# Kernel tuning notes

Hardware: AMD Instinct MI355X
Metric: run time of the kernel (lower is better)

## Reference

```python
import jax, jax.numpy as jnp
import numpy as np

N, M, D_MODEL, H, D_K, D_V = 2048, 2048, 1024, 16, 64, 64


def setup_inputs() -> dict:
    key = jax.random.key(0)
    ks = jax.random.split(key, 12)
    s = D_MODEL ** -0.5
    Q = jax.random.normal(ks[0], (N, D_MODEL), dtype=jnp.float32)
    K = jax.random.normal(ks[1], (M, D_MODEL), dtype=jnp.float32)
    V = jax.random.normal(ks[2], (M, D_MODEL), dtype=jnp.float32)
    mask = jnp.ones((N, M), dtype=bool)  # unused by the original forward
    # stacked per-head Linear params (torch Linear: y = x @ W.T + b); here stored as (H, in, out)
    Wq = jax.random.normal(ks[3], (H, D_MODEL, D_K), dtype=jnp.float32) * s
    bq = jax.random.normal(ks[4], (H, D_K), dtype=jnp.float32) * 0.01
    Wk = jax.random.normal(ks[5], (H, D_MODEL, D_K), dtype=jnp.float32) * s
    bk = jax.random.normal(ks[6], (H, D_K), dtype=jnp.float32) * 0.01
    Wv = jax.random.normal(ks[7], (H, D_MODEL, D_V), dtype=jnp.float32) * s
    bv = jax.random.normal(ks[8], (H, D_V), dtype=jnp.float32) * 0.01
    Wo = jax.random.normal(ks[9], (H * D_V, D_MODEL), dtype=jnp.float32) * ((H * D_V) ** -0.5)
    bo = jax.random.normal(ks[10], (D_MODEL,), dtype=jnp.float32) * 0.01
    return dict(Q=Q, K=K, V=V, mask=mask, Wq=Wq, bq=bq, Wk=Wk, bk=bk,
                Wv=Wv, bv=bv, Wo=Wo, bo=bo)


def reference(Q, K, V, mask, Wq, bq, Wk, bk, Wv, bv, Wo, bo):
    # per-head projections, batched over heads (h)
    Qh = jnp.einsum('nd,hdk->hnk', Q, Wq) + bq[:, None, :]  # (H, n, d_k)
    Kh = jnp.einsum('md,hdk->hmk', K, Wk) + bk[:, None, :]  # (H, m, d_k)
    Vh = jnp.einsum('md,hdv->hmv', V, Wv) + bv[:, None, :]  # (H, m, d_v)
    # faithful to source: scale d_k**-0.5 is applied AFTER the softmax
    scores = jnp.einsum('hnk,hmk->hnm', Qh, Kh)             # (H, n, m)
    attn = jax.nn.softmax(scores, axis=-1) * (D_K ** -0.5)
    heads = jnp.einsum('hnm,hmv->hnv', attn, Vh)            # (H, n, d_v)
    concat = jnp.transpose(heads, (1, 0, 2)).reshape(heads.shape[1], H * D_V)
    return concat @ Wo + bo                                  # (n, d_model)
```

## Files before the change

kernel.cpp:

```cpp
#include <hip/hip_runtime.h>

#define N_TOK 2048
#define DMODEL 1024
#define NH 16
#define DK 64
#define SOFF 48.0f

typedef __attribute__((ext_vector_type(8))) short bfrag;
typedef __attribute__((ext_vector_type(4))) float f32x4;
typedef __attribute__((ext_vector_type(16))) float f32x16;
typedef __attribute__((ext_vector_type(4))) unsigned u32x4;

__device__ __forceinline__ unsigned short f2bf(float f) {
    unsigned u = __builtin_bit_cast(unsigned, f);
    u += 0x7FFFu + ((u >> 16) & 1u);
    return (unsigned short)(u >> 16);
}
__device__ __forceinline__ float bf2f(unsigned short u) {
    unsigned x = ((unsigned)u) << 16;
    return __builtin_bit_cast(float, x);
}
__device__ __forceinline__ unsigned cvtpk(float lo, float hi) {
    unsigned r;
    asm volatile("v_cvt_pk_bf16_f32 %0, %1, %2" : "=v"(r) : "v"(lo), "v"(hi));
    return r;
}

__device__ __forceinline__ int swz(int row, int b) {
    return row * 128 + (b ^ ((row & 7) << 4));
}

__device__ __forceinline__ void gload16(const void* g, void* l) {
    __builtin_amdgcn_global_load_lds(
        (__attribute__((address_space(1))) void*)g,
        (__attribute__((address_space(3))) void*)l,
        16, 0, 0);
}

__global__ __launch_bounds__(256) void prep_kernel(
    const float* __restrict__ Qin, const float* __restrict__ Kin, const float* __restrict__ Vin,
    const float* __restrict__ Wq_, const float* __restrict__ Wk_, const float* __restrict__ Wv_,
    const float* __restrict__ Wo_,
    unsigned short* __restrict__ AhQ, unsigned short* __restrict__ AhK, unsigned short* __restrict__ AhV,
    unsigned short* __restrict__ WthQ, unsigned short* __restrict__ WthK, unsigned short* __restrict__ WthV,
    unsigned short* __restrict__ WoT)
{
    const int bid = blockIdx.x;
    const int tid = threadIdx.x;
    __shared__ float lds[64][65];

    if (bid < 3072) {
        const int z = bid >> 10, x = bid & 1023;
        const float* src = (z == 0) ? Qin : (z == 1) ? Kin : Vin;
        unsigned short* dh = (z == 0) ? AhQ : (z == 1) ? AhK : AhV;
        size_t base = ((size_t)x * 256 + tid) * 8;
        float4 a = *reinterpret_cast<const float4*>(src + base);
        float4 b = *reinterpret_cast<const float4*>(src + base + 4);
        float f[8] = {a.x, a.y, a.z, a.w, b.x, b.y, b.z, b.w};
        unsigned short hb[8];
        #pragma unroll
        for (int i = 0; i < 8; ++i) hb[i] = f2bf(f[i]);
        *reinterpret_cast<uint4*>(dh + base) = *reinterpret_cast<const uint4*>(hb);
    } else if (bid < 3840) {
        const int t = bid - 3072;
        const int z = t >> 8, rem = t & 255;
        const int h = rem >> 4, dt = rem & 15;
        const float* W = (z == 0) ? Wq_ : (z == 1) ? Wk_ : Wv_;
        unsigned short* oh = (z == 0) ? WthQ : (z == 1) ? WthK : WthV;

        {
            int rr = tid >> 2, c4 = (tid & 3) * 16;
            const float* src = W + ((size_t)h * DMODEL + dt * 64 + rr) * DK + c4;
            #pragma unroll
            for (int i = 0; i < 4; ++i) {
                float4 v = *reinterpret_cast<const float4*>(src + i * 4);
                lds[rr][c4 + i * 4 + 0] = v.x;
                lds[rr][c4 + i * 4 + 1] = v.y;
                lds[rr][c4 + i * 4 + 2] = v.z;
                lds[rr][c4 + i * 4 + 3] = v.w;
            }
        }
        __syncthreads();
        {
            int kk_ = tid >> 2, d4 = (tid & 3) * 16;
            unsigned short hb[16];
            #pragma unroll
            for (int i = 0; i < 16; ++i) hb[i] = f2bf(lds[d4 + i][kk_]);
            size_t o = (size_t)(h * 64 + kk_) * DMODEL + dt * 64 + d4;
            *reinterpret_cast<uint4*>(oh + o)     = *reinterpret_cast<const uint4*>(hb);
            *reinterpret_cast<uint4*>(oh + o + 8) = *reinterpret_cast<const uint4*>(hb + 8);
        }
    } else {
        const int t = bid - 3840;
        const int dt = t >> 4, jt = t & 15;
        {
            int rr = tid >> 2, c4 = (tid & 3) * 16;
            const float* src = Wo_ + (size_t)(dt * 64 + rr) * DMODEL + jt * 64 + c4;
            #pragma unroll
            for (int i = 0; i < 4; ++i) {
                float4 v = *reinterpret_cast<const float4*>(src + i * 4);
                lds[rr][c4 + i * 4 + 0] = v.x;
                lds[rr][c4 + i * 4 + 1] = v.y;
                lds[rr][c4 + i * 4 + 2] = v.z;
                lds[rr][c4 + i * 4 + 3] = v.w;
            }
        }
        __syncthreads();
        {
            int jj = tid >> 2, d4 = (tid & 3) * 16;
            unsigned short hb[16];
            #pragma unroll
            for (int i = 0; i < 16; ++i) hb[i] = f2bf(lds[d4 + i][jj]);
            size_t o = (size_t)(jt * 64 + jj) * DMODEL + dt * 64 + d4;
            *reinterpret_cast<uint4*>(WoT + o)     = *reinterpret_cast<const uint4*>(hb);
            *reinterpret_cast<uint4*>(WoT + o + 8) = *reinterpret_cast<const uint4*>(hb + 8);
        }
    }
}

__global__ __launch_bounds__(256) void proj_kernel(
    const unsigned short* __restrict__ AhQ, const unsigned short* __restrict__ AhK, const unsigned short* __restrict__ AhV,
    const unsigned short* __restrict__ WthQ, const unsigned short* __restrict__ WthK, const unsigned short* __restrict__ WthV,
    const float* __restrict__ bq_, const float* __restrict__ bk_, const float* __restrict__ bv_,
    unsigned short* __restrict__ Qhh,
    unsigned short* __restrict__ Khh,
    unsigned short* __restrict__ Vt)
{
    const int z = blockIdx.z;
    const unsigned short* Ah = (z == 0) ? AhK : (z == 1) ? AhQ : AhV;
    const unsigned short* Bh = (z == 0) ? WthK : (z == 1) ? WthQ : WthV;
    const float* bias = (z == 0) ? bk_ : (z == 1) ? bq_ : bv_;

    __shared__ alignas(16) unsigned char sAh[16384];
    __shared__ alignas(16) unsigned char sBh[16384];

    const int tid = threadIdx.x;
    const int lane = tid & 63;
    const int w = tid >> 6;
    const int wm = w >> 1, wn = w & 1;
    const int g = lane >> 4, li = lane & 15;

    const int row0 = blockIdx.x * 128;
    const int col0 = blockIdx.y * 128;

    f32x4 acc[4][4];
    #pragma unroll
    for (int m = 0; m < 4; ++m)
        #pragma unroll
        for (int n = 0; n < 4; ++n) acc[m][n] = f32x4{0.f, 0.f, 0.f, 0.f};

    for (int kt = 0; kt < DMODEL; kt += 64) {
        __syncthreads();
        #pragma unroll
        for (int p = 0; p < 4; ++p) {
            int chunk = p * 256 + tid;
            int r = chunk >> 3, cc = chunk & 7;
            int cs = (cc * 8) ^ ((r & 7) << 3);
            int ldso = (p * 256 + w * 64) * 16;
            gload16(Ah + (size_t)(row0 + r) * DMODEL + kt + cs, sAh + ldso);
            gload16(Bh + (size_t)(col0 + r) * DMODEL + kt + cs, sBh + ldso);
        }
        __syncthreads();

        #pragma unroll
        for (int kk = 0; kk < 2; ++kk) {
            bfrag afh[4], bfh[4];
            #pragma unroll
            for (int m = 0; m < 4; ++m)
                afh[m] = *reinterpret_cast<const bfrag*>(sAh + swz(wm * 64 + m * 16 + li, kk * 64 + g * 16));
            #pragma unroll
            for (int n = 0; n < 4; ++n)
                bfh[n] = *reinterpret_cast<const bfrag*>(sBh + swz(wn * 64 + n * 16 + li, kk * 64 + g * 16));
            #pragma unroll
            for (int m = 0; m < 4; ++m)
                #pragma unroll
                for (int n = 0; n < 4; ++n)
                    acc[m][n] = __builtin_amdgcn_mfma_f32_16x16x32_bf16(afh[m], bfh[n], acc[m][n], 0, 0, 0);
        }
    }

    #pragma unroll
    for (int m = 0; m < 4; ++m) {
        #pragma unroll
        for (int n = 0; n < 4; ++n) {
            int colg = col0 + wn * 64 + n * 16 + li;
            float bb = bias[colg];
            int hh = colg >> 6, k = colg & 63;
            int rowb = row0 + wm * 64 + m * 16 + g * 4;
            if (z == 2) {
                unsigned short vb4[4];
                #pragma unroll
                for (int r = 0; r < 4; ++r) vb4[r] = f2bf(acc[m][n][r] + bb);
                *reinterpret_cast<uint2*>(Vt + ((size_t)hh * DK + k) * N_TOK + rowb) =
                    *reinterpret_cast<const uint2*>(vb4);
            } else {
                #pragma unroll
                for (int r = 0; r < 4; ++r) {
                    size_t o = ((size_t)hh * N_TOK + rowb + r) * DK + k;
                    float val = acc[m][n][r] + bb;
                    if (z == 1) val *= 1.44269504088896f;
                    if (z == 0) Khh[o] = f2bf(val);
                    else        Qhh[o] = f2bf(val);
                }
            }
        }
    }
}

__global__ __launch_bounds__(256) void attn_kernel(
    const unsigned short* __restrict__ Qhh,
    const unsigned short* __restrict__ Khh,
    const unsigned short* __restrict__ Vt,
    unsigned short* __restrict__ Opart, float* __restrict__ lbuf)
{
    __shared__ alignas(16) unsigned char sKh[3][8192];
    __shared__ alignas(16) unsigned char sV [3][8192];

    const int bid = blockIdx.x;
    const int orig = (bid & 7) * 128 + (bid >> 3);
    const int h       = orig >> 6;
    const int quarter = (orig >> 4) & 3;
    const int qt      = orig & 15;

    const int tid  = threadIdx.x;
    const int lane = tid & 63;
    const int w    = tid >> 6;
    const int q31  = lane & 31;
    const int hi   = lane >> 5;
    const int qrow0 = qt * 128 + w * 32;

    const unsigned short* QbH = Qhh + (size_t)h * N_TOK * DK;
    const unsigned short* KbH = Khh + (size_t)h * N_TOK * DK;
    const unsigned short* Vtb = Vt  + (size_t)h * DK * N_TOK;

    bfrag bqh[4];
    #pragma unroll
    for (int d = 0; d < 4; ++d)
        bqh[d] = *reinterpret_cast<const bfrag*>(
            QbH + (size_t)(qrow0 + q31) * DK + d * 16 + hi * 8);

    f32x16 acc0 = {}, acc1 = {};
    float lrun = 0.f;

    const int tbase = quarter * (N_TOK / 4);

#define STAGE(B, T) do {                                                     \
    _Pragma("unroll")                                                        \
    for (int p_ = 0; p_ < 2; ++p_) {                                         \
        int chunk_ = p_ * 256 + w * 64 + lane;                               \
        int r_ = chunk_ >> 3;                                                \
        int cs_ = ((chunk_ & 7) * 8) ^ ((r_ & 7) << 3);                      \
        int ldso_ = (p_ * 256 + w * 64) * 16;                                \
        gload16(KbH + (size_t)((T) + r_) * DK + cs_, sKh[B] + ldso_);        \
        gload16(Vtb + (size_t)r_ * N_TOK + (T) + cs_, sV[B] + ldso_);        \
    } } while (0)

#define MKFRAG(W, PF) do {                                                   \
    _Pragma("unroll")                                                        \
    for (int kk_ = 0; kk_ < 2; ++kk_) {                                      \
        unsigned b0_ = W[4 * kk_ + 0], b1_ = W[4 * kk_ + 1];                 \
        unsigned a0_ = W[4 * kk_ + 2], a1_ = W[4 * kk_ + 3];                 \
        unsigned sb0_ = (unsigned)__shfl_xor((int)b0_, 32);                  \
        unsigned sa0_ = (unsigned)__shfl_xor((int)a0_, 32);                  \
        unsigned sb1_ = (unsigned)__shfl_xor((int)b1_, 32);                  \
        unsigned sa1_ = (unsigned)__shfl_xor((int)a1_, 32);                  \
        u32x4 t_ = { hi ? sa0_ : b0_, hi ? sa1_ : b1_,                       \
                     hi ? a0_ : sb0_, hi ? a1_ : sb1_ };                     \
        PF[kk_] = __builtin_bit_cast(bfrag, t_);                             \
    } } while (0)

    STAGE(0, tbase);

    int cur = 0;
    for (int tt = 0; tt < 8; ++tt) {
        int nxt = cur + 1; if (nxt == 3) nxt = 0;
        if (tt < 7) {
            STAGE(nxt, tbase + (tt + 1) * 64);
            asm volatile("s_waitcnt vmcnt(4)" ::: "memory");
        } else {
            asm volatile("s_waitcnt vmcnt(0)" ::: "memory");
        }
        __builtin_amdgcn_s_barrier();
        asm volatile("" ::: "memory");

        f32x16 s0, s1;
        #pragma unroll
        for (int r = 0; r < 16; ++r) { s0[r] = -SOFF; s1[r] = -SOFF; }
        __builtin_amdgcn_s_setprio(1);
        #pragma unroll
        for (int d = 0; d < 4; ++d) {
            const int bo = d * 32 + hi * 16;
            bfrag kh0 = *reinterpret_cast<const bfrag*>(sKh[cur] + swz(q31,      bo));
            bfrag kh1 = *reinterpret_cast<const bfrag*>(sKh[cur] + swz(32 + q31, bo));
            s0 = __builtin_amdgcn_mfma_f32_32x32x16_bf16(kh0, bqh[d], s0, 0, 0, 0);
            s1 = __builtin_amdgcn_mfma_f32_32x32x16_bf16(kh1, bqh[d], s1, 0, 0, 0);
        }
        __builtin_amdgcn_s_setprio(0);

        float p0[16], p1[16];
        #pragma unroll
        for (int r = 0; r < 16; ++r) p0[r] = __builtin_exp2f(s0[r]);
        #pragma unroll
        for (int r = 0; r < 16; ++r) p1[r] = __builtin_exp2f(s1[r]);
        float ps = ((p0[0] + p0[1]) + (p0[2] + p0[3])) + ((p0[4] + p0[5]) + (p0[6] + p0[7]))
                 + ((p0[8] + p0[9]) + (p0[10] + p0[11])) + ((p0[12] + p0[13]) + (p0[14] + p0[15]))
                 + ((p1[0] + p1[1]) + (p1[2] + p1[3])) + ((p1[4] + p1[5]) + (p1[6] + p1[7]))
                 + ((p1[8] + p1[9]) + (p1[10] + p1[11])) + ((p1[12] + p1[13]) + (p1[14] + p1[15]));
        ps += __shfl_xor(ps, 32);
        lrun += ps;

        unsigned w0[8], w1[8];
        #pragma unroll
        for (int j = 0; j < 8; ++j) w0[j] = cvtpk(p0[2 * j], p0[2 * j + 1]);
        #pragma unroll
        for (int j = 0; j < 8; ++j) w1[j] = cvtpk(p1[2 * j], p1[2 * j + 1]);
        bfrag pf0[2], pf1[2];
        MKFRAG(w0, pf0);
        MKFRAG(w1, pf1);

        __builtin_amdgcn_s_setprio(1);
        #pragma unroll
        for (int ks = 0; ks < 4; ++ks) {
            bfrag pb = (ks < 2) ? pf0[ks & 1] : pf1[ks & 1];
            const int bo = ks * 32 + hi * 16;
            bfrag va0 = *reinterpret_cast<const bfrag*>(sV[cur] + swz(q31,      bo));
            bfrag va1 = *reinterpret_cast<const bfrag*>(sV[cur] + swz(32 + q31, bo));
            acc0 = __builtin_amdgcn_mfma_f32_32x32x16_bf16(va0, pb, acc0, 0, 0, 0);
            acc1 = __builtin_amdgcn_mfma_f32_32x32x16_bf16(va1, pb, acc1, 0, 0, 0);
        }
        __builtin_amdgcn_s_setprio(0);
        asm volatile("" ::: "memory");
        cur = nxt;
    }
#undef STAGE
#undef MKFRAG

    const size_t idxp = (size_t)quarter * NH * N_TOK + (size_t)h * N_TOK + qrow0 + q31;
    unsigned short* op = Opart + idxp * 64;
    #pragma unroll
    for (int m = 0; m < 4; ++m) {
        uint2 wa = make_uint2(cvtpk(acc0[4 * m], acc0[4 * m + 1]),
                              cvtpk(acc0[4 * m + 2], acc0[4 * m + 3]));
        uint2 wb = make_uint2(cvtpk(acc1[4 * m], acc1[4 * m + 1]),
                              cvtpk(acc1[4 * m + 2], acc1[4 * m + 3]));
        *reinterpret_cast<uint2*>(op + 8 * m + 4 * hi)      = wa;
        *reinterpret_cast<uint2*>(op + 32 + 8 * m + 4 * hi) = wb;
    }
    if (lane < 32)
        lbuf[idxp] = lrun;
}

__global__ __launch_bounds__(256) void combine_kernel(
    const unsigned short* __restrict__ Opart, const float* __restrict__ lbuf,
    unsigned short* __restrict__ Hc)
{
    const int tid = threadIdx.x;
    const int sub = tid & 3;
    const int idx = blockIdx.x * 64 + (tid >> 2);
    const int h = idx >> 11, row = idx & 2047;
    const int QS = NH * N_TOK;

    float lsum = 0.f;
    #pragma unroll
    for (int q = 0; q < 4; ++q) lsum += lbuf[(size_t)q * QS + idx];
    float inv = 0.125f / lsum;

    float acc[16];
    #pragma unroll
    for (int i = 0; i < 16; ++i) acc[i] = 0.f;
    #pragma unroll
    for (int q = 0; q < 4; ++q) {
        const unsigned short* Oq = Opart + ((size_t)q * QS + idx) * 64 + sub * 16;
        uint4 x = *reinterpret_cast<const uint4*>(Oq);
        uint4 y = *reinterpret_cast<const uint4*>(Oq + 8);
        unsigned wds[8] = {x.x, x.y, x.z, x.w, y.x, y.y, y.z, y.w};
        #pragma unroll
        for (int j = 0; j < 8; ++j) {
            acc[2 * j]     += bf2f((unsigned short)(wds[j] & 0xFFFF));
            acc[2 * j + 1] += bf2f((unsigned short)(wds[j] >> 16));
        }
    }
    unsigned short hb[16];
    #pragma unroll
    for (int i = 0; i < 16; ++i) hb[i] = f2bf(acc[i] * inv);
    size_t o = (size_t)row * DMODEL + h * 64 + sub * 16;
    *reinterpret_cast<uint4*>(Hc + o)     = *reinterpret_cast<const uint4*>(hb);
    *reinterpret_cast<uint4*>(Hc + o + 8) = *reinterpret_cast<const uint4*>(hb + 8);
}

__global__ __launch_bounds__(256) void oproj_kernel(
    const unsigned short* __restrict__ Hc,
    const unsigned short* __restrict__ WoT,
    const float* __restrict__ bo,
    float* __restrict__ out)
{
    __shared__ alignas(16) unsigned char sA[8192];
    __shared__ alignas(16) unsigned char sB[16384];

    const int tid = threadIdx.x;
    const int lane = tid & 63;
    const int w = tid >> 6;
    const int wm = w >> 1, wn = w & 1;
    const int g = lane >> 4, li = lane & 15;
    const int row0 = blockIdx.x * 64;
    const int col0 = blockIdx.y * 128;

    f32x4 acc[2][4];
    #pragma unroll
    for (int m = 0; m < 2; ++m)
        #pragma unroll
        for (int n = 0; n < 4; ++n) acc[m][n] = f32x4{0.f, 0.f, 0.f, 0.f};

    for (int kt = 0; kt < DMODEL; kt += 64) {
        __syncthreads();
        #pragma unroll
        for (int p = 0; p < 2; ++p) {
            int chunk = p * 256 + tid;
            int r = chunk >> 3, cc = chunk & 7;
            int cs = (cc * 8) ^ ((r & 7) << 3);
            int ldso = (p * 256 + w * 64) * 16;
            gload16(Hc + (size_t)(row0 + r) * DMODEL + kt + cs, sA + ldso);
        }
        #pragma unroll
        for (int p = 0; p < 4; ++p) {
            int chunk = p * 256 + tid;
            int r = chunk >> 3, cc = chunk & 7;
            int cs = (cc * 8) ^ ((r & 7) << 3);
            int ldso = (p * 256 + w * 64) * 16;
            gload16(WoT + (size_t)(col0 + r) * DMODEL + kt + cs, sB + ldso);
        }
        __syncthreads();

        #pragma unroll
        for (int kk = 0; kk < 2; ++kk) {
            bfrag af[2], bf_[4];
            #pragma unroll
            for (int m = 0; m < 2; ++m)
                af[m] = *reinterpret_cast<const bfrag*>(sA + swz(wm * 32 + m * 16 + li, kk * 64 + g * 16));
            #pragma unroll
            for (int n = 0; n < 4; ++n)
                bf_[n] = *reinterpret_cast<const bfrag*>(sB + swz(wn * 64 + n * 16 + li, kk * 64 + g * 16));
            #pragma unroll
            for (int m = 0; m < 2; ++m)
                #pragma unroll
                for (int n = 0; n < 4; ++n)
                    acc[m][n] = __builtin_amdgcn_mfma_f32_16x16x32_bf16(af[m], bf_[n], acc[m][n], 0, 0, 0);
        }
    }

    #pragma unroll
    for (int m = 0; m < 2; ++m) {
        #pragma unroll
        for (int n = 0; n < 4; ++n) {
            int colg = col0 + wn * 64 + n * 16 + li;
            float bb = bo[colg];
            #pragma unroll
            for (int r = 0; r < 4; ++r) {
                int rowg = row0 + wm * 32 + m * 16 + g * 4 + r;
                out[(size_t)rowg * DMODEL + colg] = acc[m][n][r] + bb;
            }
        }
    }
}

extern "C" void kernel_launch(void* const* d_in, const int* in_sizes, int n_in,
                              void* d_out, int out_size, void* d_ws, size_t ws_size,
                              hipStream_t stream) {
    (void)in_sizes; (void)n_in; (void)out_size; (void)ws_size;
    const float* Q  = (const float*)d_in[0];
    const float* K  = (const float*)d_in[1];
    const float* V  = (const float*)d_in[2];
    const float* Wq = (const float*)d_in[4];
    const float* bq = (const float*)d_in[5];
    const float* Wk = (const float*)d_in[6];
    const float* bk = (const float*)d_in[7];
    const float* Wv = (const float*)d_in[8];
    const float* bv = (const float*)d_in[9];
    const float* Wo = (const float*)d_in[10];
    const float* bo = (const float*)d_in[11];
    float* out = (float*)d_out;

    const size_t ASZ = (size_t)N_TOK * DMODEL;
    const size_t WSZ = (size_t)NH * DK * DMODEL;
    const size_t HSZ = (size_t)NH * N_TOK * DK;
    unsigned short* p = (unsigned short*)d_ws;
    unsigned short* AhQ = p; p += ASZ;
    unsigned short* AhK = p; p += ASZ;
    unsigned short* AhV = p; p += ASZ;
    unsigned short* WthQ = p; p += WSZ;
    unsigned short* WthK = p; p += WSZ;
    unsigned short* WthV = p; p += WSZ;
    unsigned short* Qhh = p; p += HSZ;
    unsigned short* Khh = p; p += HSZ;
    unsigned short* Vt  = p; p += HSZ;
    unsigned short* Hc  = p; p += HSZ;
    unsigned short* WoT = p; p += ASZ / 2;

    unsigned short* Opart = (unsigned short*)d_ws;
    float* lbuf = (float*)(Opart + (size_t)4 * NH * N_TOK * 64);

    prep_kernel<<<dim3(4096), 256, 0, stream>>>(
        Q, K, V, Wq, Wk, Wv, Wo,
        AhQ, AhK, AhV, WthQ, WthK, WthV, WoT);
    proj_kernel<<<dim3(16, 8, 3), 256, 0, stream>>>(
        AhQ, AhK, AhV, WthQ, WthK, WthV,
        bq, bk, bv, Qhh, Khh, Vt);
    attn_kernel<<<dim3(1024), 256, 0, stream>>>(Qhh, Khh, Vt, Opart, lbuf);
    combine_kernel<<<dim3(512), 256, 0, stream>>>(Opart, lbuf, Hc);
    oproj_kernel<<<dim3(32, 8), 256, 0, stream>>>(Hc, WoT, bo, out);
}
```

Before: 96.95 us.

## Split attention keys into two halves instead of four, halving partial outputs

The attention kernel now splits each head's keys across two blocks instead of four. Each block runs 16 key tiles rather than 8, and the grid shrinks from 1024 to 512 blocks. The combine kernel sums two partial outputs and two row sums instead of four, which cuts partial-buffer writes and reads and gives each block longer pipelined loops. In exchange, the attention kernel has fewer blocks to spread over the 256 CUs, two per CU, which may lower occupancy and latency hiding.

After: 95.00 us (median of 2 runs). -2.0%, faster.

```diff
diff --git a/kernel.cpp b/kernel.cpp
--- a/kernel.cpp
+++ b/kernel.cpp
@@ -217,10 +217,10 @@
     __shared__ alignas(16) unsigned char sV [3][8192];
 
     const int bid = blockIdx.x;
-    const int orig = (bid & 7) * 128 + (bid >> 3);
-    const int h       = orig >> 6;
-    const int quarter = (orig >> 4) & 3;
-    const int qt      = orig & 15;
+    const int orig = (bid & 7) * 64 + (bid >> 3);
+    const int h    = orig >> 5;
+    const int half = (orig >> 4) & 1;
+    const int qt   = orig & 15;
 
     const int tid  = threadIdx.x;
     const int lane = tid & 63;
@@ -242,7 +242,7 @@
     f32x16 acc0 = {}, acc1 = {};
     float lrun = 0.f;
 
-    const int tbase = quarter * (N_TOK / 4);
+    const int tbase = half * (N_TOK / 2);
 
 #define STAGE(B, T) do {                                                     \
     _Pragma("unroll")                                                        \
@@ -272,9 +272,9 @@
     STAGE(0, tbase);
 
     int cur = 0;
-    for (int tt = 0; tt < 8; ++tt) {
+    for (int tt = 0; tt < 16; ++tt) {
         int nxt = cur + 1; if (nxt == 3) nxt = 0;
-        if (tt < 7) {
+        if (tt < 15) {
             STAGE(nxt, tbase + (tt + 1) * 64);
             asm volatile("s_waitcnt vmcnt(4)" ::: "memory");
         } else {
@@ -335,7 +335,7 @@
 #undef STAGE
 #undef MKFRAG
 
-    const size_t idxp = (size_t)quarter * NH * N_TOK + (size_t)h * N_TOK + qrow0 + q31;
+    const size_t idxp = (size_t)half * NH * N_TOK + (size_t)h * N_TOK + qrow0 + q31;
     unsigned short* op = Opart + idxp * 64;
     #pragma unroll
     for (int m = 0; m < 4; ++m) {
@@ -358,31 +358,28 @@
     const int sub = tid & 3;
     const int idx = blockIdx.x * 64 + (tid >> 2);
     const int h = idx >> 11, row = idx & 2047;
-    const int QS = NH * N_TOK;
-
-    float lsum = 0.f;
-    #pragma unroll
-    for (int q = 0; q < 4; ++q) lsum += lbuf[(size_t)q * QS + idx];
-    float inv = 0.125f / lsum;
-
-    float acc[16];
-    #pragma unroll
-    for (int i = 0; i < 16; ++i) acc[i] = 0.f;
-    #pragma unroll
-    for (int q = 0; q < 4; ++q) {
-        const unsigned short* Oq = Opart + ((size_t)q * QS + idx) * 64 + sub * 16;
-        uint4 x = *reinterpret_cast<const uint4*>(Oq);
-        uint4 y = *reinterpret_cast<const uint4*>(Oq + 8);
-        unsigned wds[8] = {x.x, x.y, x.z, x.w, y.x, y.y, y.z, y.w};
-        #pragma unroll
-        for (int j = 0; j < 8; ++j) {
-            acc[2 * j]     += bf2f((unsigned short)(wds[j] & 0xFFFF));
-            acc[2 * j + 1] += bf2f((unsigned short)(wds[j] >> 16));
-        }
-    }
+    const int HS = NH * N_TOK;
+
+    float inv = 0.125f / (lbuf[idx] + lbuf[HS + idx]);
+
+    const unsigned short* O1 = Opart + (size_t)idx * 64 + sub * 16;
+    const unsigned short* O2 = Opart + ((size_t)HS + idx) * 64 + sub * 16;
+    uint4 x1 = *reinterpret_cast<const uint4*>(O1);
+    uint4 y1 = *reinterpret_cast<const uint4*>(O1 + 8);
+    uint4 x2 = *reinterpret_cast<const uint4*>(O2);
+    uint4 y2 = *reinterpret_cast<const uint4*>(O2 + 8);
+    unsigned wa[8] = {x1.x, x1.y, x1.z, x1.w, y1.x, y1.y, y1.z, y1.w};
+    unsigned wb[8] = {x2.x, x2.y, x2.z, x2.w, y2.x, y2.y, y2.z, y2.w};
     unsigned short hb[16];
     #pragma unroll
-    for (int i = 0; i < 16; ++i) hb[i] = f2bf(acc[i] * inv);
+    for (int j = 0; j < 8; ++j) {
+        float lo = (bf2f((unsigned short)(wa[j] & 0xFFFF)) +
+                    bf2f((unsigned short)(wb[j] & 0xFFFF))) * inv;
+        float hi2 = (bf2f((unsigned short)(wa[j] >> 16)) +
+                     bf2f((unsigned short)(wb[j] >> 16))) * inv;
+        hb[2 * j]     = f2bf(lo);
+        hb[2 * j + 1] = f2bf(hi2);
+    }
     size_t o = (size_t)row * DMODEL + h * 64 + sub * 16;
     *reinterpret_cast<uint4*>(Hc + o)     = *reinterpret_cast<const uint4*>(hb);
     *reinterpret_cast<uint4*>(Hc + o + 8) = *reinterpret_cast<const uint4*>(hb + 8);
@@ -497,7 +494,7 @@
     unsigned short* WoT = p; p += ASZ / 2;
 
     unsigned short* Opart = (unsigned short*)d_ws;
-    float* lbuf = (float*)(Opart + (size_t)4 * NH * N_TOK * 64);
+    float* lbuf = (float*)(Opart + (size_t)2 * NH * N_TOK * 64);
 
     prep_kernel<<<dim3(4096), 256, 0, stream>>>(
         Q, K, V, Wq, Wk, Wv, Wo,
@@ -505,7 +502,7 @@
     proj_kernel<<<dim3(16, 8, 3), 256, 0, stream>>>(
         AhQ, AhK, AhV, WthQ, WthK, WthV,
         bq, bk, bv, Qhh, Khh, Vt);
-    attn_kernel<<<dim3(1024), 256, 0, stream>>>(Qhh, Khh, Vt, Opart, lbuf);
+    attn_kernel<<<dim3(512), 256, 0, stream>>>(Qhh, Khh, Vt, Opart, lbuf);
     combine_kernel<<<dim3(512), 256, 0, stream>>>(Opart, lbuf, Hc);
     oproj_kernel<<<dim3(32, 8), 256, 0, stream>>>(Hc, WoT, bo, out);
 }
```
